# Optimization experiments

Measured on AMD Instinct MI355X. Metric: run time of the kernel, lower is better.

Reference implementation:

```python
import jax, jax.numpy as jnp
import numpy as np


def setup_inputs() -> dict:
    key = jax.random.key(0)
    k1, k2, k3, k4, k5 = jax.random.split(key, 5)
    B, T, C, H = 4, 4096, 768, 64
    x = jax.random.normal(k1, (B, T, C), dtype=jnp.float32)
    attention_mask = jax.random.randint(k2, (B, T), 0, 2, dtype=jnp.int32)
    # Linear(embed_dim, head_size, bias=False) weights, stored as [C, H] for x @ W
    scale = 1.0 / np.sqrt(C)
    Wk = jax.random.normal(k3, (C, H), dtype=jnp.float32) * scale
    Wq = jax.random.normal(k4, (C, H), dtype=jnp.float32) * scale
    Wv = jax.random.normal(k5, (C, H), dtype=jnp.float32) * scale
    return {"x": x, "attention_mask": attention_mask, "Wk": Wk, "Wq": Wq, "Wv": Wv}


def reference(x, attention_mask, Wk, Wq, Wv):
    B, T, C = x.shape
    k = jnp.einsum("btc,ch->bth", x, Wk)   # [B,T,H]
    q = jnp.einsum("btc,ch->bth", x, Wq)   # [B,T,H]
    v = jnp.einsum("btc,ch->bth", x, Wv)   # [B,T,H]
    # NOTE: original scales by C**-0.5 (embed_dim), not head_size**-0.5
    wei = jnp.einsum("bqh,bkh->bqk", q, k) * (C ** -0.5)   # [B,T,T]
    # key-side padding mask: attention_mask [B,T] -> [B,1,T]
    wei = jnp.where(attention_mask[:, None, :] == 0, -jnp.inf, wei)
    wei = jax.nn.softmax(wei, axis=-1)
    # dropout is identity in eval mode
    out = jnp.einsum("bqk,bkh->bqh", wei, v)   # [B,T,H]
    return out
```

## Files before the change

### kernel.cpp

```cpp
#include <hip/hip_runtime.h>

#define Bn 4
#define Tn 4096
#define Cn 768
#define Hn 64
#define Mn (Bn * Tn)
#define SL2E 0.05205861629707232f

typedef __bf16 bf16x8 __attribute__((ext_vector_type(8)));
typedef float f32x4 __attribute__((ext_vector_type(4)));
typedef unsigned short us8 __attribute__((ext_vector_type(8)));

union U8 { us8 u; bf16x8 b; };

#define MFMA16(a, b, c) __builtin_amdgcn_mfma_f32_16x16x32_bf16((a), (b), (c), 0, 0, 0)

__device__ __forceinline__ unsigned short f2bf(float f) {
  unsigned u = __float_as_uint(f);
  u += 0x7fffu + ((u >> 16) & 1u);
  return (unsigned short)(u >> 16);
}

__global__ __launch_bounds__(256) void wt_prep(const float* __restrict__ Wq,
                                               const float* __restrict__ Wk,
                                               const float* __restrict__ Wv,
                                               unsigned short* __restrict__ WT) {
  int n = blockIdx.x;
  const float* src = (n < 64) ? Wq : (n < 128) ? Wk : Wv;
  int h = n & 63;
  for (int c = threadIdx.x; c < Cn; c += 256)
    WT[n * Cn + c] = f2bf(src[c * Hn + h]);
}

__global__ __launch_bounds__(256) void proj(const float* __restrict__ x,
                                            const unsigned short* __restrict__ WT,
                                            unsigned short* __restrict__ qkv) {
  __shared__ unsigned short a_lds[16 * Cn];
  int tid = threadIdx.x;
  int wv = tid >> 6, lane = tid & 63, r = lane & 15, bq = lane >> 4;
  int m0 = blockIdx.x * 16;

#pragma unroll
  for (int i = 0; i < 6; i++) {
    int q = tid + 256 * i;
    int rr = q / 96, cw = q % 96;
    const float* p = x + (long)(m0 + rr) * Cn + cw * 8;
    f32x4 f0 = *(const f32x4*)p;
    f32x4 f1 = *(const f32x4*)(p + 4);
    us8 uu;
    uu[0] = f2bf(f0[0]); uu[1] = f2bf(f0[1]); uu[2] = f2bf(f0[2]); uu[3] = f2bf(f0[3]);
    uu[4] = f2bf(f1[0]); uu[5] = f2bf(f1[1]); uu[6] = f2bf(f1[2]); uu[7] = f2bf(f1[3]);
    *(us8*)&a_lds[rr * Cn + ((cw * 8) ^ ((rr & 7) << 3))] = uu;
  }
  __syncthreads();

  f32x4 acc[3];
#pragma unroll
  for (int nt = 0; nt < 3; nt++) acc[nt] = (f32x4){0.f, 0.f, 0.f, 0.f};

  int n0 = wv * 48;
  int sw = (r & 7) << 3;
  for (int kc = 0; kc < 12; kc++) {
    U8 a0, a1;
    a0.u = *(const us8*)&a_lds[r * Cn + kc * 64 + ((bq * 8) ^ sw)];
    a1.u = *(const us8*)&a_lds[r * Cn + kc * 64 + ((32 + bq * 8) ^ sw)];
#pragma unroll
    for (int nt = 0; nt < 3; nt++) {
      const unsigned short* wp = WT + (long)(n0 + nt * 16 + r) * Cn + kc * 64 + bq * 8;
      U8 b0, b1;
      b0.u = *(const us8*)wp;
      b1.u = *(const us8*)(wp + 32);
      acc[nt] = MFMA16(a0.b, b0.b, acc[nt]);
      acc[nt] = MFMA16(a1.b, b1.b, acc[nt]);
    }
  }
#pragma unroll
  for (int nt = 0; nt < 3; nt++) {
    int col = n0 + nt * 16 + r;
    unsigned short* outp = qkv + (long)(col >> 6) * Mn * Hn;
    int ncol = col & 63;
#pragma unroll
    for (int j = 0; j < 4; j++) {
      int m = m0 + bq * 4 + j;
      outp[(long)m * Hn + ncol] = f2bf(acc[nt][j]);
    }
  }
}

#define LSTR 72

__global__ __launch_bounds__(256) void attn(const unsigned short* __restrict__ qkv,
                                            const int* __restrict__ amask,
                                            float* __restrict__ pacc,
                                            float* __restrict__ pl,
                                            int span) {
  __shared__ unsigned short K_lds[64 * LSTR];
  __shared__ unsigned short VT_lds[64 * LSTR];
  __shared__ unsigned short P_lds[64 * LSTR];

  int tid = threadIdx.x;
  int wv = tid >> 6, lane = tid & 63, r = lane & 15, bq = lane >> 4;
  int qt = blockIdx.x, bidx = blockIdx.y, sp = blockIdx.z;
  int q0 = qt * 64;
  long base = (long)bidx * Tn;

  const unsigned short* q_ws = qkv;
  const unsigned short* k_ws = qkv + (long)Mn * Hn;
  const unsigned short* v_ws = qkv + 2L * Mn * Hn;

  U8 qf[2];
  {
    const unsigned short* qp = q_ws + (base + q0 + wv * 16 + r) * Hn + bq * 8;
    qf[0].u = *(const us8*)qp;
    qf[1].u = *(const us8*)(qp + 32);
  }

  float lrun[4];
  f32x4 acc[4];
#pragma unroll
  for (int j = 0; j < 4; j++) lrun[j] = 0.f;
#pragma unroll
  for (int nt = 0; nt < 4; nt++) acc[nt] = (f32x4){0.f, 0.f, 0.f, 0.f};

  int kv_beg = sp * span, kv_end = kv_beg + span;
  int srow = tid >> 3, scb = tid & 7;

  us8 kpref0, kpref1, vpref0, vpref1;
  int mpref;
  {
    const unsigned short* kb = k_ws + (base + kv_beg) * Hn;
    const unsigned short* vb = v_ws + (base + kv_beg) * Hn;
    kpref0 = *(const us8*)(kb + srow * Hn + scb * 8);
    kpref1 = *(const us8*)(kb + (srow + 32) * Hn + scb * 8);
    vpref0 = *(const us8*)(vb + srow * Hn + scb * 8);
    vpref1 = *(const us8*)(vb + (srow + 32) * Hn + scb * 8);
    mpref = amask[base + kv_beg + lane];
  }

  for (int kv0 = kv_beg; kv0 < kv_end; kv0 += 64) {
    __syncthreads();
    *(us8*)&K_lds[srow * LSTR + scb * 8] = kpref0;
    *(us8*)&K_lds[(srow + 32) * LSTR + scb * 8] = kpref1;
    {
      int xr0 = srow ^ (scb << 3);
      int xr1 = (srow + 32) ^ (scb << 3);
#pragma unroll
      for (int e = 0; e < 8; e++) {
        VT_lds[(scb * 8 + e) * LSTR + xr0] = vpref0[e];
        VT_lds[(scb * 8 + e) * LSTR + xr1] = vpref1[e];
      }
    }
    unsigned long long mb = __ballot(mpref != 0);
    __syncthreads();

    if (kv0 + 64 < kv_end) {
      const unsigned short* kb = k_ws + (base + kv0 + 64) * Hn;
      const unsigned short* vb = v_ws + (base + kv0 + 64) * Hn;
      kpref0 = *(const us8*)(kb + srow * Hn + scb * 8);
      kpref1 = *(const us8*)(kb + (srow + 32) * Hn + scb * 8);
      vpref0 = *(const us8*)(vb + srow * Hn + scb * 8);
      vpref1 = *(const us8*)(vb + (srow + 32) * Hn + scb * 8);
      mpref = amask[base + kv0 + 64 + lane];
    }

    f32x4 s[4];
#pragma unroll
    for (int kt = 0; kt < 4; kt++) {
      const unsigned short* kp = &K_lds[(kt * 16 + r) * LSTR + bq * 8];
      U8 b0, b1;
      b0.u = *(const us8*)kp;
      b1.u = *(const us8*)(kp + 32);
      f32x4 z = (f32x4){0.f, 0.f, 0.f, 0.f};
      z = MFMA16(qf[0].b, b0.b, z);
      z = MFMA16(qf[1].b, b1.b, z);
      s[kt] = z;
    }

    float ps[4] = {0.f, 0.f, 0.f, 0.f};
#pragma unroll
    for (int kt = 0; kt < 4; kt++) {
      bool live = (mb >> (kt * 16 + r)) & 1ull;
#pragma unroll
      for (int j = 0; j < 4; j++) {
        float p = live ? exp2f(s[kt][j] * SL2E) : 0.f;
        s[kt][j] = p;
        ps[j] += p;
      }
    }
#pragma unroll
    for (int j = 0; j < 4; j++) {
      ps[j] += __shfl_xor(ps[j], 1);
      ps[j] += __shfl_xor(ps[j], 2);
      ps[j] += __shfl_xor(ps[j], 4);
      ps[j] += __shfl_xor(ps[j], 8);
      lrun[j] += ps[j];
    }

#pragma unroll
    for (int kt = 0; kt < 4; kt++)
#pragma unroll
      for (int j = 0; j < 4; j++)
        P_lds[(wv * 16 + bq * 4 + j) * LSTR + kt * 16 + r] = f2bf(s[kt][j]);

    U8 pa0, pa1;
    const unsigned short* pp = &P_lds[(wv * 16 + r) * LSTR + bq * 8];
    pa0.u = *(const us8*)pp;
    pa1.u = *(const us8*)(pp + 32);
#pragma unroll
    for (int nt = 0; nt < 4; nt++) {
      int col = nt * 16 + r;
      int sw = (col >> 3) << 3;
      U8 v0, v1;
      v0.u = *(const us8*)&VT_lds[col * LSTR + ((bq * 8) ^ sw)];
      v1.u = *(const us8*)&VT_lds[col * LSTR + ((32 + bq * 8) ^ sw)];
      acc[nt] = MFMA16(pa0.b, v0.b, acc[nt]);
      acc[nt] = MFMA16(pa1.b, v1.b, acc[nt]);
    }
  }

  long pb = ((long)sp * Bn + bidx) * 64 + qt;
  float* accp = pacc + pb * 4096;
#pragma unroll
  for (int nt = 0; nt < 4; nt++)
#pragma unroll
    for (int j = 0; j < 4; j++)
      accp[(wv * 16 + bq * 4 + j) * 64 + nt * 16 + r] = acc[nt][j];
  if (r == 0) {
#pragma unroll
    for (int j = 0; j < 4; j++)
      pl[pb * 64 + wv * 16 + bq * 4 + j] = lrun[j];
  }
}

__global__ __launch_bounds__(256) void merge(const float* __restrict__ pacc,
                                             const float* __restrict__ pl,
                                             float* __restrict__ out, int S) {
  int qt = blockIdx.x, bidx = blockIdx.y;
  int tid = threadIdx.x;
  int row = tid >> 2, c0 = (tid & 3) * 16;

  float L = 0.f;
  f32x4 o[4];
#pragma unroll
  for (int c = 0; c < 4; c++) o[c] = (f32x4){0.f, 0.f, 0.f, 0.f};
  for (int s = 0; s < S; s++) {
    long pb = ((long)s * Bn + bidx) * 64 + qt;
    L += pl[pb * 64 + row];
    const float* ap = pacc + pb * 4096 + row * 64 + c0;
#pragma unroll
    for (int c = 0; c < 4; c++) {
      f32x4 a = *(const f32x4*)(ap + c * 4);
#pragma unroll
      for (int e = 0; e < 4; e++) o[c][e] += a[e];
    }
  }
  float rl = L > 0.f ? 1.f / L : 0.f;
  float* op = out + ((long)bidx * Tn + qt * 64 + row) * 64 + c0;
#pragma unroll
  for (int c = 0; c < 4; c++) {
    f32x4 v;
#pragma unroll
    for (int e = 0; e < 4; e++) v[e] = o[c][e] * rl;
    *(f32x4*)(op + c * 4) = v;
  }
}

extern "C" void kernel_launch(void* const* d_in, const int* in_sizes, int n_in,
                              void* d_out, int out_size, void* d_ws, size_t ws_size,
                              hipStream_t stream) {
  const float* x  = (const float*)d_in[0];
  const int* am   = (const int*)d_in[1];
  const float* Wk = (const float*)d_in[2];
  const float* Wq = (const float*)d_in[3];
  const float* Wv = (const float*)d_in[4];
  float* out = (float*)d_out;

  size_t off_wt   = 0;
  size_t off_qkv  = off_wt + (size_t)192 * Cn * 2;
  size_t off_pacc = off_qkv + (size_t)3 * Mn * Hn * 2;
  size_t per_split = (size_t)Bn * 64 * 4096 * 4 + (size_t)Bn * 64 * 64 * 4;
  int S = 8;
  while (S > 1 && off_pacc + (size_t)S * per_split > ws_size) S >>= 1;
  size_t acc_bytes = (size_t)S * Bn * 64 * 4096 * 4;

  unsigned short* WT  = (unsigned short*)((char*)d_ws + off_wt);
  unsigned short* qkv = (unsigned short*)((char*)d_ws + off_qkv);
  float* pacc = (float*)((char*)d_ws + off_pacc);
  float* pl   = (float*)((char*)d_ws + off_pacc + acc_bytes);

  wt_prep<<<192, 256, 0, stream>>>(Wq, Wk, Wv, WT);
  proj<<<Mn / 16, 256, 0, stream>>>(x, WT, qkv);
  attn<<<dim3(Tn / 64, Bn, S), 256, 0, stream>>>(qkv, am, pacc, pl, Tn / S);
  merge<<<dim3(64, Bn), 256, 0, stream>>>(pacc, pl, out, S);
}
```

Before: 183.1 us.

## Enlarge projection M-tile, widen merge grid, use hardware bf16 conversion

The projection kernel now handles 32 rows per block instead of 16, so each weight fragment loaded from global memory feeds two MFMA row tiles. This halves weight traffic per output row, at the cost of doubling LDS to 48KB per block and adding more accumulator registers. The merge kernel is split into four blocks per 64-row tile with one float4 per thread, giving more blocks and more memory parallelism. The manual rounding routine is replaced by the compiler's native bf16 cast.

Measured after the change: 167.3 us. 8.6% less time.

```diff
diff --git a/kernel.cpp b/kernel.cpp
--- a/kernel.cpp
+++ b/kernel.cpp
@@ -15,10 +15,9 @@
 
 #define MFMA16(a, b, c) __builtin_amdgcn_mfma_f32_16x16x32_bf16((a), (b), (c), 0, 0, 0)
 
-__device__ __forceinline__ unsigned short f2bf(float f) {
-  unsigned u = __float_as_uint(f);
-  u += 0x7fffu + ((u >> 16) & 1u);
-  return (unsigned short)(u >> 16);
+__device__ __forceinline__ unsigned short cvt_bf(float f) {
+  __bf16 h = (__bf16)f;
+  return *(unsigned short*)&h;
 }
 
 __global__ __launch_bounds__(256) void wt_prep(const float* __restrict__ Wq,
@@ -29,62 +28,75 @@
   const float* src = (n < 64) ? Wq : (n < 128) ? Wk : Wv;
   int h = n & 63;
   for (int c = threadIdx.x; c < Cn; c += 256)
-    WT[n * Cn + c] = f2bf(src[c * Hn + h]);
+    WT[n * Cn + c] = cvt_bf(src[c * Hn + h]);
 }
 
 __global__ __launch_bounds__(256) void proj(const float* __restrict__ x,
                                             const unsigned short* __restrict__ WT,
                                             unsigned short* __restrict__ qkv) {
-  __shared__ unsigned short a_lds[16 * Cn];
+  __shared__ unsigned short a_lds[32 * Cn];
   int tid = threadIdx.x;
   int wv = tid >> 6, lane = tid & 63, r = lane & 15, bq = lane >> 4;
-  int m0 = blockIdx.x * 16;
-
-#pragma unroll
-  for (int i = 0; i < 6; i++) {
+  int m0 = blockIdx.x * 32;
+
+#pragma unroll
+  for (int i = 0; i < 12; i++) {
     int q = tid + 256 * i;
     int rr = q / 96, cw = q % 96;
     const float* p = x + (long)(m0 + rr) * Cn + cw * 8;
     f32x4 f0 = *(const f32x4*)p;
     f32x4 f1 = *(const f32x4*)(p + 4);
     us8 uu;
-    uu[0] = f2bf(f0[0]); uu[1] = f2bf(f0[1]); uu[2] = f2bf(f0[2]); uu[3] = f2bf(f0[3]);
-    uu[4] = f2bf(f1[0]); uu[5] = f2bf(f1[1]); uu[6] = f2bf(f1[2]); uu[7] = f2bf(f1[3]);
+    uu[0] = cvt_bf(f0[0]); uu[1] = cvt_bf(f0[1]); uu[2] = cvt_bf(f0[2]); uu[3] = cvt_bf(f0[3]);
+    uu[4] = cvt_bf(f1[0]); uu[5] = cvt_bf(f1[1]); uu[6] = cvt_bf(f1[2]); uu[7] = cvt_bf(f1[3]);
     *(us8*)&a_lds[rr * Cn + ((cw * 8) ^ ((rr & 7) << 3))] = uu;
   }
   __syncthreads();
 
-  f32x4 acc[3];
-#pragma unroll
-  for (int nt = 0; nt < 3; nt++) acc[nt] = (f32x4){0.f, 0.f, 0.f, 0.f};
+  f32x4 acc[2][3];
+#pragma unroll
+  for (int mt = 0; mt < 2; mt++)
+#pragma unroll
+    for (int nt = 0; nt < 3; nt++) acc[mt][nt] = (f32x4){0.f, 0.f, 0.f, 0.f};
 
   int n0 = wv * 48;
-  int sw = (r & 7) << 3;
+#pragma unroll
   for (int kc = 0; kc < 12; kc++) {
-    U8 a0, a1;
-    a0.u = *(const us8*)&a_lds[r * Cn + kc * 64 + ((bq * 8) ^ sw)];
-    a1.u = *(const us8*)&a_lds[r * Cn + kc * 64 + ((32 + bq * 8) ^ sw)];
+    U8 a[2][2];
+#pragma unroll
+    for (int mt = 0; mt < 2; mt++) {
+      int rr = mt * 16 + r;
+      int sw = (rr & 7) << 3;
+#pragma unroll
+      for (int ks = 0; ks < 2; ks++)
+        a[mt][ks].u = *(const us8*)&a_lds[rr * Cn + kc * 64 + ((ks * 32 + bq * 8) ^ sw)];
+    }
 #pragma unroll
     for (int nt = 0; nt < 3; nt++) {
       const unsigned short* wp = WT + (long)(n0 + nt * 16 + r) * Cn + kc * 64 + bq * 8;
       U8 b0, b1;
       b0.u = *(const us8*)wp;
       b1.u = *(const us8*)(wp + 32);
-      acc[nt] = MFMA16(a0.b, b0.b, acc[nt]);
-      acc[nt] = MFMA16(a1.b, b1.b, acc[nt]);
-    }
-  }
-#pragma unroll
-  for (int nt = 0; nt < 3; nt++) {
-    int col = n0 + nt * 16 + r;
-    unsigned short* outp = qkv + (long)(col >> 6) * Mn * Hn;
-    int ncol = col & 63;
-#pragma unroll
-    for (int j = 0; j < 4; j++) {
-      int m = m0 + bq * 4 + j;
-      outp[(long)m * Hn + ncol] = f2bf(acc[nt][j]);
-    }
-  }
+#pragma unroll
+      for (int mt = 0; mt < 2; mt++) {
+        acc[mt][nt] = MFMA16(a[mt][0].b, b0.b, acc[mt][nt]);
+        acc[mt][nt] = MFMA16(a[mt][1].b, b1.b, acc[mt][nt]);
+      }
+    }
+  }
+#pragma unroll
+  for (int mt = 0; mt < 2; mt++)
+#pragma unroll
+    for (int nt = 0; nt < 3; nt++) {
+      int col = n0 + nt * 16 + r;
+      unsigned short* outp = qkv + (long)(col >> 6) * Mn * Hn;
+      int ncol = col & 63;
+#pragma unroll
+      for (int j = 0; j < 4; j++) {
+        int m = m0 + mt * 16 + bq * 4 + j;
+        outp[(long)m * Hn + ncol] = cvt_bf(acc[mt][nt][j]);
+      }
+    }
 }
 
 #define LSTR 72
@@ -200,7 +212,7 @@
     for (int kt = 0; kt < 4; kt++)
 #pragma unroll
       for (int j = 0; j < 4; j++)
-        P_lds[(wv * 16 + bq * 4 + j) * LSTR + kt * 16 + r] = f2bf(s[kt][j]);
+        P_lds[(wv * 16 + bq * 4 + j) * LSTR + kt * 16 + r] = cvt_bf(s[kt][j]);
 
     U8 pa0, pa1;
     const unsigned short* pp = &P_lds[(wv * 16 + r) * LSTR + bq * 8];
@@ -235,34 +247,26 @@
 __global__ __launch_bounds__(256) void merge(const float* __restrict__ pacc,
                                              const float* __restrict__ pl,
                                              float* __restrict__ out, int S) {
-  int qt = blockIdx.x, bidx = blockIdx.y;
+  int g = blockIdx.x, bidx = blockIdx.y;
+  int qt = g >> 2, sub = g & 3;
   int tid = threadIdx.x;
-  int row = tid >> 2, c0 = (tid & 3) * 16;
+  int row = sub * 16 + (tid >> 4);
+  int c0 = (tid & 15) * 4;
 
   float L = 0.f;
-  f32x4 o[4];
-#pragma unroll
-  for (int c = 0; c < 4; c++) o[c] = (f32x4){0.f, 0.f, 0.f, 0.f};
+  f32x4 o = (f32x4){0.f, 0.f, 0.f, 0.f};
   for (int s = 0; s < S; s++) {
     long pb = ((long)s * Bn + bidx) * 64 + qt;
     L += pl[pb * 64 + row];
-    const float* ap = pacc + pb * 4096 + row * 64 + c0;
-#pragma unroll
-    for (int c = 0; c < 4; c++) {
-      f32x4 a = *(const f32x4*)(ap + c * 4);
-#pragma unroll
-      for (int e = 0; e < 4; e++) o[c][e] += a[e];
-    }
+    f32x4 a = *(const f32x4*)(pacc + pb * 4096 + row * 64 + c0);
+#pragma unroll
+    for (int e = 0; e < 4; e++) o[e] += a[e];
   }
   float rl = L > 0.f ? 1.f / L : 0.f;
-  float* op = out + ((long)bidx * Tn + qt * 64 + row) * 64 + c0;
-#pragma unroll
-  for (int c = 0; c < 4; c++) {
-    f32x4 v;
-#pragma unroll
-    for (int e = 0; e < 4; e++) v[e] = o[c][e] * rl;
-    *(f32x4*)(op + c * 4) = v;
-  }
+  f32x4 v;
+#pragma unroll
+  for (int e = 0; e < 4; e++) v[e] = o[e] * rl;
+  *(f32x4*)(out + ((long)bidx * Tn + qt * 64 + row) * 64 + c0) = v;
 }
 
 extern "C" void kernel_launch(void* const* d_in, const int* in_sizes, int n_in,
@@ -289,7 +293,7 @@
   float* pl   = (float*)((char*)d_ws + off_pacc + acc_bytes);
 
   wt_prep<<<192, 256, 0, stream>>>(Wq, Wk, Wv, WT);
-  proj<<<Mn / 16, 256, 0, stream>>>(x, WT, qkv);
+  proj<<<Mn / 32, 256, 0, stream>>>(x, WT, qkv);
   attn<<<dim3(Tn / 64, Bn, S), 256, 0, stream>>>(qkv, am, pacc, pl, Tn / S);
-  merge<<<dim3(64, Bn), 256, 0, stream>>>(pacc, pl, out, S);
-}
+  merge<<<dim3(Tn / 16, Bn), 256, 0, stream>>>(pacc, pl, out, S);
+}
```
